# Kernel optimization log

Hardware: AMD Instinct MI355X
Metric: run time of the kernel (lower is better)

## Reference

```python
import jax, jax.numpy as jnp
import numpy as np

B, V, R, K = 256, 10475, 75, 5  # batch, vertices, regions, verts per region


def setup_inputs() -> dict:
    key = jax.random.key(0)
    k1, k2, k3 = jax.random.split(key, 3)
    v1 = jax.random.normal(k1, (B, V, 3), dtype=jnp.float32)
    v2 = jax.random.normal(k2, (B, V, 3), dtype=jnp.float32)
    rid_to_vid_list = jax.random.randint(k3, (R, K), 0, V, dtype=jnp.int64)
    return {"v1": v1, "v2": v2, "rid_to_vid_list": rid_to_vid_list}


def reference(v1, v2, rid_to_vid_list):
    # Gather region vertices: [B, R, K, 3]
    g1 = v1[:, rid_to_vid_list, :]
    g2 = v2[:, rid_to_vid_list, :]
    # Squared norms per gathered point: [B, R, K]
    rx = jnp.sum(g1 * g1, axis=-1)
    ry = jnp.sum(g2 * g2, axis=-1)
    # Cross terms for all region pairs: [B, R, R, K, K]
    zz = jnp.einsum("bipd,bjqd->bijpq", g1, g2)
    P = rx[:, :, None, :, None] + ry[:, None, :, None, :] - 2.0 * zz
    # Original: clamp, sqrt, then min over the K*K pair distances
    d = jnp.sqrt(jnp.clip(P, 0.0, None))
    heatmap = jnp.min(d.reshape(d.shape[0], d.shape[1], d.shape[2], -1), axis=3)
    return heatmap
```

## Files before the change

kernel.cpp:

```cpp
#include <hip/hip_runtime.h>

#define BB 256
#define VV 10475
#define RR 75
#define KK 5
#define RKN (RR * KK)
#define NOUT (RR * RR)
#define TPB 1024

__global__ __launch_bounds__(TPB) void ContactMap_47691316854895_kernel(
    const float* __restrict__ v1,
    const float* __restrict__ v2,
    const int* __restrict__ rid,
    float* __restrict__ out)
{
    __shared__ float g1s[RKN * 3];
    __shared__ float g2s[RKN * 3];

    const int b = blockIdx.x;
    const float* v1b = v1 + (size_t)b * VV * 3;
    const float* v2b = v2 + (size_t)b * VV * 3;

    if (threadIdx.x < RKN) {
        const int t = threadIdx.x;
        const int idx = rid[t];
        const float* p1 = v1b + (size_t)idx * 3;
        const float* p2 = v2b + (size_t)idx * 3;
        g1s[t * 3 + 0] = p1[0];
        g1s[t * 3 + 1] = p1[1];
        g1s[t * 3 + 2] = p1[2];
        g2s[t * 3 + 0] = p2[0];
        g2s[t * 3 + 1] = p2[1];
        g2s[t * 3 + 2] = p2[2];
    }
    __syncthreads();

    float* outb = out + (size_t)b * NOUT;

    for (int e = threadIdx.x; e < NOUT; e += TPB) {
        const int i = e / RR;
        const int j = e % RR;

        float ax[KK], ay[KK], az[KK];
#pragma unroll
        for (int p = 0; p < KK; ++p) {
            ax[p] = g1s[(i * KK + p) * 3 + 0];
            ay[p] = g1s[(i * KK + p) * 3 + 1];
            az[p] = g1s[(i * KK + p) * 3 + 2];
        }

        float best = 3.402823466e+38f;
#pragma unroll
        for (int q = 0; q < KK; ++q) {
            const float bx = g2s[(j * KK + q) * 3 + 0];
            const float by = g2s[(j * KK + q) * 3 + 1];
            const float bz = g2s[(j * KK + q) * 3 + 2];
#pragma unroll
            for (int p = 0; p < KK; ++p) {
                const float dx = ax[p] - bx;
                const float dy = ay[p] - by;
                const float dz = az[p] - bz;
                const float d2 = dx * dx + dy * dy + dz * dz;
                best = fminf(best, d2);
            }
        }
        outb[e] = sqrtf(best);
    }
}

extern "C" void kernel_launch(void* const* d_in, const int* in_sizes, int n_in,
                              void* d_out, int out_size, void* d_ws, size_t ws_size,
                              hipStream_t stream) {
    const float* v1 = (const float*)d_in[0];
    const float* v2 = (const float*)d_in[1];
    const int* rid = (const int*)d_in[2];
    float* out = (float*)d_out;

    ContactMap_47691316854895_kernel<<<dim3(BB), dim3(TPB), 0, stream>>>(v1, v2, rid, out);
}
```

Baseline: 15.15 us.

## Register-tile 3x3 region pairs per thread and pad shared points to float4

Each thread now computes a 3x3 tile of region pairs, holding the i-side points in registers and reusing the j-side points across three rows. This cuts shared-memory loads per output and replaces the strided loop over outputs with a fixed 625-thread mapping. Shared points are padded to float4 so each point is one vector load. Per-thread stores become strided within the tile, which may hurt write coalescing, and fewer threads are active per block.

```diff
diff --git a/kernel.cpp b/kernel.cpp
--- a/kernel.cpp
+++ b/kernel.cpp
@@ -1,4 +1,5 @@
 #include <hip/hip_runtime.h>
+#include <float.h>
 
 #define BB 256
 #define VV 10475
@@ -6,7 +7,12 @@
 #define KK 5
 #define RKN (RR * KK)
 #define NOUT (RR * RR)
-#define TPB 1024
+#define TI 3
+#define TJ 3
+#define NTI (RR / TI)
+#define NTJ (RR / TJ)
+#define NTILE (NTI * NTJ)
+#define TPB 640
 
 __global__ __launch_bounds__(TPB) void ContactMap_47691316854895_kernel(
     const float* __restrict__ v1,
@@ -14,57 +20,64 @@
     const int* __restrict__ rid,
     float* __restrict__ out)
 {
-    __shared__ float g1s[RKN * 3];
-    __shared__ float g2s[RKN * 3];
+    __shared__ float4 g1s[RKN];
+    __shared__ float4 g2s[RKN];
 
     const int b = blockIdx.x;
+    const int tid = threadIdx.x;
     const float* v1b = v1 + (size_t)b * VV * 3;
     const float* v2b = v2 + (size_t)b * VV * 3;
 
-    if (threadIdx.x < RKN) {
-        const int t = threadIdx.x;
-        const int idx = rid[t];
+    if (tid < RKN) {
+        const int idx = rid[tid];
         const float* p1 = v1b + (size_t)idx * 3;
         const float* p2 = v2b + (size_t)idx * 3;
-        g1s[t * 3 + 0] = p1[0];
-        g1s[t * 3 + 1] = p1[1];
-        g1s[t * 3 + 2] = p1[2];
-        g2s[t * 3 + 0] = p2[0];
-        g2s[t * 3 + 1] = p2[1];
-        g2s[t * 3 + 2] = p2[2];
+        g1s[tid] = make_float4(p1[0], p1[1], p1[2], 0.0f);
+        g2s[tid] = make_float4(p2[0], p2[1], p2[2], 0.0f);
     }
     __syncthreads();
 
+    if (tid >= NTILE) return;
+
+    const int i0 = (tid / NTJ) * TI;
+    const int j0 = (tid % NTJ) * TJ;
+
+    float ax[TI][KK], ay[TI][KK], az[TI][KK];
+#pragma unroll
+    for (int ii = 0; ii < TI; ++ii) {
+#pragma unroll
+        for (int p = 0; p < KK; ++p) {
+            const float4 a = g1s[(i0 + ii) * KK + p];
+            ax[ii][p] = a.x; ay[ii][p] = a.y; az[ii][p] = a.z;
+        }
+    }
+
     float* outb = out + (size_t)b * NOUT;
 
-    for (int e = threadIdx.x; e < NOUT; e += TPB) {
-        const int i = e / RR;
-        const int j = e % RR;
-
-        float ax[KK], ay[KK], az[KK];
 #pragma unroll
-        for (int p = 0; p < KK; ++p) {
-            ax[p] = g1s[(i * KK + p) * 3 + 0];
-            ay[p] = g1s[(i * KK + p) * 3 + 1];
-            az[p] = g1s[(i * KK + p) * 3 + 2];
-        }
-
-        float best = 3.402823466e+38f;
+    for (int jj = 0; jj < TJ; ++jj) {
+        float bx[KK], by[KK], bz[KK];
 #pragma unroll
         for (int q = 0; q < KK; ++q) {
-            const float bx = g2s[(j * KK + q) * 3 + 0];
-            const float by = g2s[(j * KK + q) * 3 + 1];
-            const float bz = g2s[(j * KK + q) * 3 + 2];
+            const float4 v = g2s[(j0 + jj) * KK + q];
+            bx[q] = v.x; by[q] = v.y; bz[q] = v.z;
+        }
+#pragma unroll
+        for (int ii = 0; ii < TI; ++ii) {
+            float best = FLT_MAX;
 #pragma unroll
             for (int p = 0; p < KK; ++p) {
-                const float dx = ax[p] - bx;
-                const float dy = ay[p] - by;
-                const float dz = az[p] - bz;
-                const float d2 = dx * dx + dy * dy + dz * dz;
-                best = fminf(best, d2);
+#pragma unroll
+                for (int q = 0; q < KK; ++q) {
+                    const float dx = ax[ii][p] - bx[q];
+                    const float dy = ay[ii][p] - by[q];
+                    const float dz = az[ii][p] - bz[q];
+                    const float d2 = dx * dx + dy * dy + dz * dz;
+                    best = fminf(best, d2);
+                }
             }
+            outb[(size_t)(i0 + ii) * RR + (j0 + jj)] = sqrtf(best);
         }
-        outb[e] = sqrtf(best);
     }
 }
 
```

Measured after the change: 14.39 us. 5.0% less time.
